# Optimization experiments

Measured on AMD Instinct MI355X. Metric: run time of the kernel, lower is better.

The kernel has to match this reference:

```python
import jax, jax.numpy as jnp
import numpy as np

N = 50000
E = 600000
D = 128
BN_EPS = 1e-5
GIN_EPS = 0.0  # init_eps=0, not learned


def setup_inputs() -> dict:
    key = jax.random.key(0)
    ks = jax.random.split(key, 8)
    x = jax.random.normal(ks[0], (N, D), dtype=jnp.float32)
    edge_index = jax.random.randint(ks[1], (2, E), 0, N, dtype=jnp.int64)
    s = 1.0 / np.sqrt(D)
    w1 = jax.random.uniform(ks[2], (D, D), jnp.float32, -s, s)
    b1 = jax.random.uniform(ks[3], (D,), jnp.float32, -s, s)
    w2 = jax.random.uniform(ks[4], (D, D), jnp.float32, -s, s)
    b2 = jax.random.uniform(ks[5], (D,), jnp.float32, -s, s)
    gamma = jnp.ones((D,), jnp.float32)
    beta = jnp.zeros((D,), jnp.float32)
    return {"x": x, "edge_index": edge_index, "w1": w1, "b1": b1,
            "w2": w2, "b2": b2, "gamma": gamma, "beta": beta}


def reference(x, edge_index, w1, b1, w2, b2, gamma, beta):
    src, dst = edge_index[0], edge_index[1]
    # GINConv sum aggregation: out[i] = sum_{(j,i) in E} x[j]
    agg = jax.ops.segment_sum(x[src], dst, num_segments=N)  # [N, D]
    h = (1.0 + GIN_EPS) * x + agg
    # 2-layer MLP (Linear-ReLU-Linear)
    h = jax.nn.relu(h @ w1 + b1)
    h = h @ w2 + b2
    # training-mode BatchNorm over nodes (biased variance)
    mean = jnp.mean(h, axis=0)
    var = jnp.var(h, axis=0)
    h = (h - mean) * jax.lax.rsqrt(var + BN_EPS) * gamma + beta
    h = jax.nn.relu(h)
    # residual (in_dim == out_dim); dropout p=0.0 -> identity
    return x + h
```

## Files before the change

### kernel.cpp

```cpp
#include <hip/hip_runtime.h>

#define NN 50000
#define EE 600000
#define DD 128
#define MTILE 128
#define LDSTR 136
#define MAXDEG 64
#define NSLICE 32

typedef __attribute__((ext_vector_type(8))) short short8;
typedef __attribute__((ext_vector_type(4))) float f32x4;

static __device__ __forceinline__ unsigned short f2bf(float f) {
    unsigned int u = __float_as_uint(f);
    u += 0x7FFF + ((u >> 16) & 1);
    return (unsigned short)(u >> 16);
}
static __device__ __forceinline__ float bflo(unsigned int u) {
    return __uint_as_float(u << 16);
}
static __device__ __forceinline__ float bfhi(unsigned int u) {
    return __uint_as_float(u & 0xFFFF0000u);
}


__global__ __launch_bounds__(256) void k_prep(const float* __restrict__ w1,
                                              const float* __restrict__ w2,
                                              const float* __restrict__ x,
                                              const int* __restrict__ ei,
                                              int* __restrict__ cursor,
                                              int* __restrict__ srcPad,
                                              unsigned short* __restrict__ wt,
                                              unsigned int* __restrict__ xb) {
    int tid = blockIdx.x * 256 + threadIdx.x;
    if (tid < EE) {
        int s = ei[tid];
        int d = ei[EE + tid];
        int pos = atomicAdd(&cursor[d], 1);
        if (pos < MAXDEG) srcPad[(d << 6) + pos] = s;
    }
    if (tid < 32768) {
        int w = tid >> 14, idx = tid & 16383;
        int k = idx >> 7, n = idx & 127;
        const float* src = w ? w2 : w1;
        wt[w * 16384 + n * 128 + k] = f2bf(src[k * 128 + n]);
    }
    int xi = tid - 32768;
    if (xi >= 0 && xi < NN * DD / 2) {
        float2 v = ((const float2*)x)[xi];
        xb[xi] = (unsigned int)f2bf(v.x) | ((unsigned int)f2bf(v.y) << 16);
    }
}


__global__ __launch_bounds__(256) void k_agg(const unsigned int* __restrict__ xb,
                                             const int* __restrict__ cursor,
                                             const int* srcPad,
                                             unsigned int* h0) {
    int wave = (blockIdx.x * blockDim.x + threadIdx.x) >> 6;
    int lane = threadIdx.x & 63;
    if (wave >= NN) return;
    int cnt = cursor[wave];
    if (cnt > MAXDEG) cnt = MAXDEG;
    int sv = srcPad[(wave << 6) + lane];
    unsigned int self = xb[(wave << 6) + lane];
    float ax = bflo(self), ay = bfhi(self);
    int j = 0;
    for (; j + 8 <= cnt; j += 8) {
        int a0 = __shfl(sv, j, 64),     a1 = __shfl(sv, j + 1, 64);
        int a2 = __shfl(sv, j + 2, 64), a3 = __shfl(sv, j + 3, 64);
        int a4 = __shfl(sv, j + 4, 64), a5 = __shfl(sv, j + 5, 64);
        int a6 = __shfl(sv, j + 6, 64), a7 = __shfl(sv, j + 7, 64);
        unsigned int u0 = xb[(a0 << 6) + lane], u1 = xb[(a1 << 6) + lane];
        unsigned int u2 = xb[(a2 << 6) + lane], u3 = xb[(a3 << 6) + lane];
        unsigned int u4 = xb[(a4 << 6) + lane], u5 = xb[(a5 << 6) + lane];
        unsigned int u6 = xb[(a6 << 6) + lane], u7 = xb[(a7 << 6) + lane];
        ax += bflo(u0) + bflo(u1) + bflo(u2) + bflo(u3)
            + bflo(u4) + bflo(u5) + bflo(u6) + bflo(u7);
        ay += bfhi(u0) + bfhi(u1) + bfhi(u2) + bfhi(u3)
            + bfhi(u4) + bfhi(u5) + bfhi(u6) + bfhi(u7);
    }
    for (; j + 4 <= cnt; j += 4) {
        int a0 = __shfl(sv, j, 64),     a1 = __shfl(sv, j + 1, 64);
        int a2 = __shfl(sv, j + 2, 64), a3 = __shfl(sv, j + 3, 64);
        unsigned int u0 = xb[(a0 << 6) + lane], u1 = xb[(a1 << 6) + lane];
        unsigned int u2 = xb[(a2 << 6) + lane], u3 = xb[(a3 << 6) + lane];
        ax += bflo(u0) + bflo(u1) + bflo(u2) + bflo(u3);
        ay += bfhi(u0) + bfhi(u1) + bfhi(u2) + bfhi(u3);
    }
    for (; j < cnt; ++j) {
        int s = __shfl(sv, j, 64);
        unsigned int u = xb[(s << 6) + lane];
        ax += bflo(u);
        ay += bfhi(u);
    }
    h0[(wave << 6) + lane] = (unsigned int)f2bf(ax) | ((unsigned int)f2bf(ay) << 16);
}


__global__ __launch_bounds__(256) void k_gemm(const unsigned short* __restrict__ A,
                                              const unsigned short* __restrict__ W,
                                              const float* __restrict__ bias,
                                              unsigned short* __restrict__ Cb,
                                              float* __restrict__ priv,
                                              int relu) {
    __shared__ __align__(16) unsigned short As[MTILE * LDSTR];
    __shared__ __align__(16) unsigned short Ws[128 * LDSTR];
    int t = threadIdx.x;
    int row0 = blockIdx.x * MTILE;

    #pragma unroll
    for (int i = 0; i < 8; ++i) {
        int idx = i * 256 + t;
        int r = idx >> 4, c = idx & 15;
        *(short8*)&Ws[r * LDSTR + c * 8] = *(const short8*)&W[r * 128 + c * 8];
    }
    #pragma unroll
    for (int i = 0; i < 8; ++i) {
        int idx = i * 256 + t;
        int r = idx >> 4, c = idx & 15;
        int gr = row0 + r;
        short8 v = (short8)0;
        if (gr < NN) v = *(const short8*)&A[gr * 128 + c * 8];
        *(short8*)&As[r * LDSTR + c * 8] = v;
    }
    __syncthreads();

    int lane = t & 63, wid = t >> 6;
    int m = lane & 15, quad = lane >> 4;
    f32x4 acc[2][8];
    #pragma unroll
    for (int mt = 0; mt < 2; ++mt)
        #pragma unroll
        for (int i = 0; i < 8; ++i) acc[mt][i] = (f32x4)0.f;

    #pragma unroll
    for (int kc = 0; kc < 4; ++kc) {
        int ko = kc * 32 + quad * 8;
        short8 af0 = *(const short8*)&As[(wid * 32 + m) * LDSTR + ko];
        short8 af1 = *(const short8*)&As[(wid * 32 + 16 + m) * LDSTR + ko];
        #pragma unroll
        for (int nt = 0; nt < 8; ++nt) {
            short8 bfr = *(const short8*)&Ws[(nt * 16 + m) * LDSTR + ko];
            acc[0][nt] = __builtin_amdgcn_mfma_f32_16x16x32_bf16(af0, bfr, acc[0][nt], 0, 0, 0);
            acc[1][nt] = __builtin_amdgcn_mfma_f32_16x16x32_bf16(af1, bfr, acc[1][nt], 0, 0, 0);
        }
    }

    if (relu) {
        #pragma unroll
        for (int nt = 0; nt < 8; ++nt) {
            int col = nt * 16 + m;
            float bv = bias[col];
            #pragma unroll
            for (int mt = 0; mt < 2; ++mt)
                #pragma unroll
                for (int r = 0; r < 4; ++r) {
                    int gr = row0 + wid * 32 + mt * 16 + quad * 4 + r;
                    if (gr < NN) Cb[gr * 128 + col] = f2bf(fmaxf(acc[mt][nt][r] + bv, 0.f));
                }
        }
    } else {
        float* myslice = priv + ((blockIdx.x * 4 + wid) & (NSLICE - 1)) * 2 * DD;
        #pragma unroll
        for (int nt = 0; nt < 8; ++nt) {
            int col = nt * 16 + m;
            float bv = bias[col];
            float s = 0.f, sq = 0.f;
            #pragma unroll
            for (int mt = 0; mt < 2; ++mt)
                #pragma unroll
                for (int r = 0; r < 4; ++r) {
                    int gr = row0 + wid * 32 + mt * 16 + quad * 4 + r;
                    if (gr < NN) {
                        float v = acc[mt][nt][r] + bv;
                        Cb[gr * 128 + col] = f2bf(v);
                        s += v;
                        sq += v * v;
                    }
                }
            s  += __shfl_down(s, 32, 64);  sq += __shfl_down(sq, 32, 64);
            s  += __shfl_down(s, 16, 64);  sq += __shfl_down(sq, 16, 64);
            if (quad == 0) {
                atomicAdd(&myslice[col], s);
                atomicAdd(&myslice[DD + col], sq);
            }
        }
    }
}


__global__ __launch_bounds__(256) void k_final(const float* __restrict__ x,
                                               const unsigned int* __restrict__ h2,
                                               float* __restrict__ out,
                                               const float* __restrict__ priv,
                                               const float* __restrict__ gamma,
                                               const float* __restrict__ beta) {
    __shared__ float ssc[DD], ssh[DD];
    int t = threadIdx.x;
    if (t < DD) {
        float s = 0.f, sq = 0.f;
        #pragma unroll
        for (int sl = 0; sl < NSLICE; ++sl) {
            s  += priv[sl * 2 * DD + t];
            sq += priv[sl * 2 * DD + DD + t];
        }
        float mean = s * (1.0f / NN);
        float var = fmaxf(sq * (1.0f / NN) - mean * mean, 0.f);
        float sc = gamma[t] * rsqrtf(var + 1e-5f);
        ssc[t] = sc;
        ssh[t] = beta[t] - mean * sc;
    }
    __syncthreads();
    #pragma unroll
    for (int u = 0; u < 4; ++u) {
        int idx = blockIdx.x * 1024 + u * 256 + t;
        if (idx >= NN * DD / 4) return;
        int c0 = (idx & 31) * 4;
        unsigned int p0 = h2[2 * idx];
        unsigned int p1 = h2[2 * idx + 1];
        float4 xv = ((const float4*)x)[idx];
        float4 o;
        o.x = xv.x + fmaxf(fmaf(bflo(p0), ssc[c0 + 0], ssh[c0 + 0]), 0.f);
        o.y = xv.y + fmaxf(fmaf(bfhi(p0), ssc[c0 + 1], ssh[c0 + 1]), 0.f);
        o.z = xv.z + fmaxf(fmaf(bflo(p1), ssc[c0 + 2], ssh[c0 + 2]), 0.f);
        o.w = xv.w + fmaxf(fmaf(bfhi(p1), ssc[c0 + 3], ssh[c0 + 3]), 0.f);
        ((float4*)out)[idx] = o;
    }
}

extern "C" void kernel_launch(void* const* d_in, const int* in_sizes, int n_in,
                              void* d_out, int out_size, void* d_ws, size_t ws_size,
                              hipStream_t stream) {
    (void)in_sizes; (void)n_in; (void)out_size; (void)ws_size;
    const float* x     = (const float*)d_in[0];
    const int*   ei    = (const int*)d_in[1];
    const float* w1    = (const float*)d_in[2];
    const float* b1    = (const float*)d_in[3];
    const float* w2    = (const float*)d_in[4];
    const float* b2    = (const float*)d_in[5];
    const float* gamma = (const float*)d_in[6];
    const float* beta  = (const float*)d_in[7];
    float* out = (float*)d_out;

    char* wsb = (char*)d_ws;
    int*   cursor  = (int*)(wsb);
    int*   srcPad  = (int*)(wsb + 0x40000);
    unsigned int*   h0w = (unsigned int*)srcPad;
    unsigned short* h0b = (unsigned short*)srcPad;
    unsigned short* h2b = (unsigned short*)srcPad;
    unsigned int*   h2w = (unsigned int*)srcPad;
    unsigned int*   xb  = (unsigned int*)(wsb + 0xD00000);
    unsigned short* h1b = (unsigned short*)xb;
    unsigned short* wt  = (unsigned short*)(wsb + 0x1940000);
    float* priv    = (float*)(wsb + 0x1960000);

    (void)hipMemsetAsync(cursor, 0, NN * sizeof(int), stream);
    (void)hipMemsetAsync(priv, 0, NSLICE * 2 * DD * sizeof(float), stream);

    k_prep<<<(32768 + NN * DD / 2 + 255) / 256, 256, 0, stream>>>(w1, w2, x, ei, cursor, srcPad, wt, xb);
    k_agg<<<(NN * 64 + 255) / 256, 256, 0, stream>>>(xb, cursor, srcPad, h0w);
    k_gemm<<<(NN + MTILE - 1) / MTILE, 256, 0, stream>>>(h0b, wt, b1, h1b, nullptr, 1);
    k_gemm<<<(NN + MTILE - 1) / MTILE, 256, 0, stream>>>(h1b, wt + 16384, b2, h2b, priv, 0);
    k_final<<<(NN * DD / 4 + 1023) / 1024, 256, 0, stream>>>(x, h2w, out, priv, gamma, beta);
}
```

Baseline: 202.2 us.

## Drop LDS staging in GEMM, store padded neighbor lists as 16-bit indices

The GEMM kernel no longer stages A and W tiles through shared memory behind a barrier. Each wave now loads its own 32 rows of A and the W fragments straight from global memory into registers, processing W in two halves. Padded source indices are stored as 16-bit values, which is valid because N is below 65536, and each prep thread now handles 4 edges. The workspace is re-laid out so h0 no longer aliases srcPad. The aim is to cut index-buffer traffic and remove LDS and barrier overhead, at the cost of every wave re-reading the full weight matrix through cache.

```diff
diff --git a/kernel.cpp b/kernel.cpp
--- a/kernel.cpp
+++ b/kernel.cpp
@@ -3,10 +3,9 @@
 #define NN 50000
 #define EE 600000
 #define DD 128
-#define MTILE 128
-#define LDSTR 136
 #define MAXDEG 64
 #define NSLICE 32
+#define EPT 4
 
 typedef __attribute__((ext_vector_type(8))) short short8;
 typedef __attribute__((ext_vector_type(4))) float f32x4;
@@ -29,15 +28,19 @@
                                               const float* __restrict__ x,
                                               const int* __restrict__ ei,
                                               int* __restrict__ cursor,
-                                              int* __restrict__ srcPad,
+                                              unsigned short* __restrict__ srcPad,
                                               unsigned short* __restrict__ wt,
                                               unsigned int* __restrict__ xb) {
     int tid = blockIdx.x * 256 + threadIdx.x;
-    if (tid < EE) {
-        int s = ei[tid];
-        int d = ei[EE + tid];
-        int pos = atomicAdd(&cursor[d], 1);
-        if (pos < MAXDEG) srcPad[(d << 6) + pos] = s;
+    if (tid < EE / EPT) {
+        #pragma unroll
+        for (int i = 0; i < EPT; ++i) {
+            int e = tid + i * (EE / EPT);
+            int s = ei[e];
+            int d = ei[EE + e];
+            int pos = atomicAdd(&cursor[d], 1);
+            if (pos < MAXDEG) srcPad[(d << 6) + pos] = (unsigned short)s;
+        }
     }
     if (tid < 32768) {
         int w = tid >> 14, idx = tid & 16383;
@@ -55,8 +58,8 @@
 
 __global__ __launch_bounds__(256) void k_agg(const unsigned int* __restrict__ xb,
                                              const int* __restrict__ cursor,
-                                             const int* srcPad,
-                                             unsigned int* h0) {
+                                             const unsigned short* __restrict__ srcPad,
+                                             unsigned int* __restrict__ h0) {
     int wave = (blockIdx.x * blockDim.x + threadIdx.x) >> 6;
     int lane = threadIdx.x & 63;
     if (wave >= NN) return;
@@ -104,30 +107,22 @@
                                               unsigned short* __restrict__ Cb,
                                               float* __restrict__ priv,
                                               int relu) {
-    __shared__ __align__(16) unsigned short As[MTILE * LDSTR];
-    __shared__ __align__(16) unsigned short Ws[128 * LDSTR];
-    int t = threadIdx.x;
-    int row0 = blockIdx.x * MTILE;
-
-    #pragma unroll
-    for (int i = 0; i < 8; ++i) {
-        int idx = i * 256 + t;
-        int r = idx >> 4, c = idx & 15;
-        *(short8*)&Ws[r * LDSTR + c * 8] = *(const short8*)&W[r * 128 + c * 8];
-    }
-    #pragma unroll
-    for (int i = 0; i < 8; ++i) {
-        int idx = i * 256 + t;
-        int r = idx >> 4, c = idx & 15;
-        int gr = row0 + r;
-        short8 v = (short8)0;
-        if (gr < NN) v = *(const short8*)&A[gr * 128 + c * 8];
-        *(short8*)&As[r * LDSTR + c * 8] = v;
-    }
-    __syncthreads();
-
-    int lane = t & 63, wid = t >> 6;
+    int wave = (blockIdx.x * 256 + threadIdx.x) >> 6;
+    int lane = threadIdx.x & 63;
     int m = lane & 15, quad = lane >> 4;
+    int row0 = wave * 32;
+    if (row0 >= NN) return;
+
+    short8 af[2][4];
+    #pragma unroll
+    for (int mt = 0; mt < 2; ++mt) {
+        int gr = row0 + mt * 16 + m;
+        #pragma unroll
+        for (int kc = 0; kc < 4; ++kc)
+            af[mt][kc] = (gr < NN) ? *(const short8*)&A[gr * 128 + kc * 32 + quad * 8]
+                                   : (short8)0;
+    }
+
     f32x4 acc[2][8];
     #pragma unroll
     for (int mt = 0; mt < 2; ++mt)
@@ -135,16 +130,20 @@
         for (int i = 0; i < 8; ++i) acc[mt][i] = (f32x4)0.f;
 
     #pragma unroll
-    for (int kc = 0; kc < 4; ++kc) {
-        int ko = kc * 32 + quad * 8;
-        short8 af0 = *(const short8*)&As[(wid * 32 + m) * LDSTR + ko];
-        short8 af1 = *(const short8*)&As[(wid * 32 + 16 + m) * LDSTR + ko];
-        #pragma unroll
-        for (int nt = 0; nt < 8; ++nt) {
-            short8 bfr = *(const short8*)&Ws[(nt * 16 + m) * LDSTR + ko];
-            acc[0][nt] = __builtin_amdgcn_mfma_f32_16x16x32_bf16(af0, bfr, acc[0][nt], 0, 0, 0);
-            acc[1][nt] = __builtin_amdgcn_mfma_f32_16x16x32_bf16(af1, bfr, acc[1][nt], 0, 0, 0);
-        }
+    for (int h = 0; h < 2; ++h) {
+        short8 wf[4][4];
+        #pragma unroll
+        for (int nt = 0; nt < 4; ++nt)
+            #pragma unroll
+            for (int kc = 0; kc < 4; ++kc)
+                wf[nt][kc] = *(const short8*)&W[(h * 64 + nt * 16 + m) * 128 + kc * 32 + quad * 8];
+        #pragma unroll
+        for (int kc = 0; kc < 4; ++kc)
+            #pragma unroll
+            for (int nt = 0; nt < 4; ++nt) {
+                acc[0][h * 4 + nt] = __builtin_amdgcn_mfma_f32_16x16x32_bf16(af[0][kc], wf[nt][kc], acc[0][h * 4 + nt], 0, 0, 0);
+                acc[1][h * 4 + nt] = __builtin_amdgcn_mfma_f32_16x16x32_bf16(af[1][kc], wf[nt][kc], acc[1][h * 4 + nt], 0, 0, 0);
+            }
     }
 
     if (relu) {
@@ -156,12 +155,12 @@
             for (int mt = 0; mt < 2; ++mt)
                 #pragma unroll
                 for (int r = 0; r < 4; ++r) {
-                    int gr = row0 + wid * 32 + mt * 16 + quad * 4 + r;
+                    int gr = row0 + mt * 16 + quad * 4 + r;
                     if (gr < NN) Cb[gr * 128 + col] = f2bf(fmaxf(acc[mt][nt][r] + bv, 0.f));
                 }
         }
     } else {
-        float* myslice = priv + ((blockIdx.x * 4 + wid) & (NSLICE - 1)) * 2 * DD;
+        float* myslice = priv + (wave & (NSLICE - 1)) * 2 * DD;
         #pragma unroll
         for (int nt = 0; nt < 8; ++nt) {
             int col = nt * 16 + m;
@@ -171,7 +170,7 @@
             for (int mt = 0; mt < 2; ++mt)
                 #pragma unroll
                 for (int r = 0; r < 4; ++r) {
-                    int gr = row0 + wid * 32 + mt * 16 + quad * 4 + r;
+                    int gr = row0 + mt * 16 + quad * 4 + r;
                     if (gr < NN) {
                         float v = acc[mt][nt][r] + bv;
                         Cb[gr * 128 + col] = f2bf(v);
@@ -244,23 +243,23 @@
     float* out = (float*)d_out;
 
     char* wsb = (char*)d_ws;
-    int*   cursor  = (int*)(wsb);
-    int*   srcPad  = (int*)(wsb + 0x40000);
-    unsigned int*   h0w = (unsigned int*)srcPad;
-    unsigned short* h0b = (unsigned short*)srcPad;
-    unsigned short* h2b = (unsigned short*)srcPad;
-    unsigned int*   h2w = (unsigned int*)srcPad;
-    unsigned int*   xb  = (unsigned int*)(wsb + 0xD00000);
-    unsigned short* h1b = (unsigned short*)xb;
-    unsigned short* wt  = (unsigned short*)(wsb + 0x1940000);
-    float* priv    = (float*)(wsb + 0x1960000);
+    int*            cursor = (int*)(wsb);
+    unsigned short* srcPad = (unsigned short*)(wsb + 0x40000);
+    unsigned int*   xb     = (unsigned int*)(wsb + 0x680000);
+    unsigned short* h1b    = (unsigned short*)xb;
+    unsigned int*   h0w    = (unsigned int*)(wsb + 0x1300000);
+    unsigned short* h0b    = (unsigned short*)h0w;
+    unsigned short* h2b    = (unsigned short*)h0w;
+    unsigned int*   h2w    = (unsigned int*)h0w;
+    unsigned short* wt     = (unsigned short*)(wsb + 0x1F80000);
+    float*          priv   = (float*)(wsb + 0x1FA0000);
 
     (void)hipMemsetAsync(cursor, 0, NN * sizeof(int), stream);
     (void)hipMemsetAsync(priv, 0, NSLICE * 2 * DD * sizeof(float), stream);
 
     k_prep<<<(32768 + NN * DD / 2 + 255) / 256, 256, 0, stream>>>(w1, w2, x, ei, cursor, srcPad, wt, xb);
     k_agg<<<(NN * 64 + 255) / 256, 256, 0, stream>>>(xb, cursor, srcPad, h0w);
-    k_gemm<<<(NN + MTILE - 1) / MTILE, 256, 0, stream>>>(h0b, wt, b1, h1b, nullptr, 1);
-    k_gemm<<<(NN + MTILE - 1) / MTILE, 256, 0, stream>>>(h1b, wt + 16384, b2, h2b, priv, 0);
+    k_gemm<<<(NN + 127) / 128, 256, 0, stream>>>(h0b, wt, b1, h1b, nullptr, 1);
+    k_gemm<<<(NN + 127) / 128, 256, 0, stream>>>(h1b, wt + 16384, b2, h2b, priv, 0);
     k_final<<<(NN * DD / 4 + 1023) / 1024, 256, 0, stream>>>(x, h2w, out, priv, gamma, beta);
 }
```

Result: faster. 192.9 us (-4.6%).
